# Performance work log

Measured on AMD Instinct MI355X. Metric: run time of the kernel, lower is better.

Reference implementation:

```python
import jax, jax.numpy as jnp
import numpy as np

N_NODES = 50000
N_EDGES = 800000
NODE_DIM = 128
HIDDEN = 256
LATENT = 128
COND = 5


def setup_inputs() -> dict:
    key = jax.random.key(0)
    ks = jax.random.split(key, 10)
    s = lambda d: 1.0 / np.sqrt(d)
    return {
        "node_features": jax.random.normal(ks[0], (N_NODES, NODE_DIM), jnp.float32),
        "conditions": jax.random.normal(ks[1], (COND,), jnp.float32),
        "src": jax.random.randint(ks[2], (N_EDGES,), 0, N_NODES, jnp.int32),
        "dst": jax.random.randint(ks[3], (N_EDGES,), 0, N_NODES, jnp.int32),
        "W1": jax.random.normal(ks[4], (NODE_DIM, HIDDEN), jnp.float32) * s(NODE_DIM),
        "b1": jnp.zeros((HIDDEN,), jnp.float32),
        "W2": jax.random.normal(ks[5], (HIDDEN, HIDDEN), jnp.float32) * s(HIDDEN),
        "b2": jnp.zeros((HIDDEN,), jnp.float32),
        "Wfc": jax.random.normal(ks[6], (HIDDEN + COND, LATENT), jnp.float32) * s(HIDDEN + COND),
        "bfc": jnp.zeros((LATENT,), jnp.float32),
        "Wmean": jax.random.normal(ks[7], (LATENT, LATENT), jnp.float32) * s(LATENT),
        "bmean": jnp.zeros((LATENT,), jnp.float32),
        "Wlogvar": jax.random.normal(ks[8], (LATENT, LATENT), jnp.float32) * s(LATENT),
        "blogvar": jnp.zeros((LATENT,), jnp.float32),
    }


def _graph_conv(x, src, dst, W, b, n_nodes):
    # gather source-node features along edges, sum-aggregate onto targets,
    # then linear transform: standard GraphConv (sum aggregation)
    agg = jax.ops.segment_sum(x[src], dst, num_segments=n_nodes)  # [N, d]
    return agg @ W + b


def reference(node_features, conditions, src, dst,
              W1, b1, W2, b2, Wfc, bfc, Wmean, bmean, Wlogvar, blogvar):
    n = node_features.shape[0]
    x = jax.nn.relu(_graph_conv(node_features, src, dst, W1, b1, n))  # [N, H]
    x = jax.nn.relu(_graph_conv(x, src, dst, W2, b2, n))              # [N, H]
    pooled = jnp.mean(x, axis=0)                                      # [H]
    h = jax.nn.relu(jnp.concatenate([pooled, conditions], axis=-1) @ Wfc + bfc)
    z_mean = h @ Wmean + bmean
    z_logvar = h @ Wlogvar + blogvar
    return z_mean, z_logvar
```

## Files before the change

kernel.cpp:

```cpp
#include <hip/hip_runtime.h>

#define N_NODES   50000
#define N_EDGES   800000
#define NODE_DIM  128
#define HIDDEN    256
#define LATENT    128
#define COND      5

#define NB        196
#define P1_CHUNK  4096
#define P1_GRID   ((N_EDGES + P1_CHUNK - 1) / P1_CHUNK)

typedef unsigned int uint;
typedef unsigned short ushort;
typedef unsigned char uchar;

typedef __attribute__((ext_vector_type(8))) short bf16x8;
typedef __attribute__((ext_vector_type(4))) float f32x4;

static __device__ __forceinline__ ushort f32_to_bf16(float f) {
    union { float f; uint u; } v; v.f = f;
    uint r = v.u + 0x7FFF + ((v.u >> 16) & 1);
    return (ushort)(r >> 16);
}
static __device__ __forceinline__ uint pack_bf16(float lo, float hi) {
    return (uint)f32_to_bf16(lo) | ((uint)f32_to_bf16(hi) << 16);
}

static __device__ __forceinline__ void gload_lds16(const void* g, void* l) {
    __builtin_amdgcn_global_load_lds(
        (const __attribute__((address_space(1))) unsigned int*)(unsigned long long)(uintptr_t)g,
        (__attribute__((address_space(3))) unsigned int*)(unsigned int)(uintptr_t)l,
        16, 0, 0);
}


#if __has_builtin(__builtin_amdgcn_cvt_pk_f32_fp8) && __has_builtin(__builtin_amdgcn_cvt_pk_fp8_f32)
#define HW_FP8 1
#endif

#ifndef HW_FP8
static __device__ __forceinline__ float dec1_fp8(uint b) {
    uint sgn = b & 0x80, mag = b & 0x7f;
    float v;
    if (mag >= 8) {
        union { uint u; float f; } t;
        t.u = (((mag >> 3) + 120) << 23) | ((mag & 7) << 20);
        v = t.f;
    } else {
        v = (float)mag * 0.001953125f;
    }
    return sgn ? -v : v;
}
static __device__ __forceinline__ uchar enc1_fp8(float f) {
    float a = fabsf(f);
    uint s = (f < 0.f) ? 0x80u : 0u;
    if (!(a >= 0.015625f)) {
        int q = (int)(a * 512.f + 0.5f);
        if (q > 7) q = 7;
        return (uchar)(s | (uint)q);
    }
    if (a >= 448.f) return (uchar)(s | 0x7E);
    union { float f; uint u; } t; t.f = a;
    uint e = (t.u >> 23) - 120;
    uint m = (t.u >> 20) & 7;
    uint rem = t.u & 0xFFFFF;
    uint v = (e << 3) | m;
    if (rem > 0x80000 || (rem == 0x80000 && (v & 1))) v++;
    if (v > 0x7E) v = 0x7E;
    return (uchar)(s | v);
}
#endif

static __device__ __forceinline__ void dec4_add(uint u, float* acc) {
#ifdef HW_FP8
    auto lo = __builtin_amdgcn_cvt_pk_f32_fp8((int)u, false);
    auto hi = __builtin_amdgcn_cvt_pk_f32_fp8((int)u, true);
    acc[0] += lo[0]; acc[1] += lo[1]; acc[2] += hi[0]; acc[3] += hi[1];
#else
    acc[0] += dec1_fp8(u & 0xff);
    acc[1] += dec1_fp8((u >> 8) & 0xff);
    acc[2] += dec1_fp8((u >> 16) & 0xff);
    acc[3] += dec1_fp8(u >> 24);
#endif
}
static __device__ __forceinline__ void dec2_add(uint u, float* acc) {
#ifdef HW_FP8
    auto lo = __builtin_amdgcn_cvt_pk_f32_fp8((int)u, false);
    acc[0] += lo[0]; acc[1] += lo[1];
#else
    acc[0] += dec1_fp8(u & 0xff);
    acc[1] += dec1_fp8((u >> 8) & 0xff);
#endif
}
static __device__ __forceinline__ uint enc2_fp8(float a, float b) {
#ifdef HW_FP8
    return (uint)__builtin_amdgcn_cvt_pk_fp8_f32(a, b, 0, false) & 0xFFFFu;
#else
    return (uint)enc1_fp8(a) | ((uint)enc1_fp8(b) << 8);
#endif
}
static __device__ __forceinline__ uchar enc1(float v) {
#ifdef HW_FP8
    return (uchar)(__builtin_amdgcn_cvt_pk_fp8_f32(v, v, 0, false) & 0xff);
#else
    return enc1_fp8(v);
#endif
}


#define NF4   (N_NODES * NODE_DIM / 4)
#define PREP1 (NF4 + NODE_DIM * HIDDEN)
#define PREP2 (PREP1 + HIDDEN * HIDDEN)
#define PREP3 (PREP2 + HIDDEN)
#define PREP4 (PREP3 + NB)
#define PREP5 (PREP4 + NB)
#define PREP6 (PREP5 + 1)

__global__ void prep_kernel(const float* __restrict__ nf,
                            const float* __restrict__ W1, const float* __restrict__ W2,
                            uchar* __restrict__ nf_fp8,
                            ushort* __restrict__ Wst1, ushort* __restrict__ Wst2,
                            float* __restrict__ pooled,
                            int* __restrict__ bcount, int* __restrict__ bcursor2,
                            int* __restrict__ hcnt) {
    int id = blockIdx.x * blockDim.x + threadIdx.x;
    if (id < NF4) {
        float4 v = reinterpret_cast<const float4*>(nf)[id];
        uint w = enc2_fp8(v.x, v.y) | (enc2_fp8(v.z, v.w) << 16);
        reinterpret_cast<uint*>(nf_fp8)[id] = w;
    } else if (id < PREP1) {
        int i = id - NF4;
        int k = i >> 8, c = i & 255;
        int idx = ((((k >> 5) * 16) + (((k & 31) >> 3) * 4 + (c >> 6))) * 64 + (c & 63)) * 8 + (k & 7);
        Wst1[idx] = f32_to_bf16(W1[i]);
    } else if (id < PREP2) {
        int i = id - PREP1;
        int k = i >> 8, c = i & 255;
        int idx = ((((k >> 5) * 16) + (((k & 31) >> 3) * 4 + (c >> 6))) * 64 + (c & 63)) * 8 + (k & 7);
        Wst2[idx] = f32_to_bf16(W2[i]);
    } else if (id < PREP3) {
        pooled[id - PREP2] = 0.f;
    } else if (id < PREP4) {
        bcount[id - PREP3] = 0;
    } else if (id < PREP5) {
        bcursor2[id - PREP4] = 0;
    } else if (id < PREP6) {
        hcnt[0] = 0;
    }
}


__global__ __launch_bounds__(256) void bcount_kernel(const int* __restrict__ dst,
                                                     int* __restrict__ bcount) {
    __shared__ int cnt[NB];
    const int t = threadIdx.x;
    for (int i = t; i < NB; i += 256) cnt[i] = 0;
    __syncthreads();
    const int base = blockIdx.x * P1_CHUNK;
#pragma unroll
    for (int i = 0; i < 16; ++i) {
        int e = base + i * 256 + t;
        if (e < N_EDGES) atomicAdd(&cnt[dst[e] >> 8], 1);
    }
    __syncthreads();
    for (int i = t; i < NB; i += 256)
        if (cnt[i] > 0) atomicAdd(&bcount[i], cnt[i]);
}

__global__ __launch_bounds__(256) void bwrite_kernel(const int* __restrict__ src,
                                                     const int* __restrict__ dst,
                                                     const int* __restrict__ bcount,
                                                     int* __restrict__ bcursor2,
                                                     uint* __restrict__ pair_buf) {
    __shared__ int s[256];
    __shared__ int cnt[NB];
    __shared__ int gbase[NB];
    const int t = threadIdx.x;
    s[t] = (t < NB) ? bcount[t] : 0;
    __syncthreads();
    for (int off = 1; off < 256; off <<= 1) {
        int v = (t >= off) ? s[t - off] : 0;
        __syncthreads();
        s[t] += v;
        __syncthreads();
    }
    for (int i = t; i < NB; i += 256) cnt[i] = 0;
    __syncthreads();

    const int base = blockIdx.x * P1_CHUNK;
    uint pk[16];
    int  bk[16], lr[16];
    bool ok[16];
#pragma unroll
    for (int i = 0; i < 16; ++i) {
        int e = base + i * 256 + t;
        ok[i] = e < N_EDGES;
        if (ok[i]) {
            int sv = src[e], d = dst[e];
            pk[i] = (uint)sv | ((uint)d << 16);
            bk[i] = d >> 8;
        }
    }
#pragma unroll
    for (int i = 0; i < 16; ++i)
        if (ok[i]) lr[i] = atomicAdd(&cnt[bk[i]], 1);
    __syncthreads();
    if (t < NB) {
        int c = cnt[t];
        if (c > 0) gbase[t] = ((t > 0) ? s[t - 1] : 0) + atomicAdd(&bcursor2[t], c);
    }
    __syncthreads();
#pragma unroll
    for (int i = 0; i < 16; ++i)
        if (ok[i]) pair_buf[gbase[bk[i]] + lr[i]] = pk[i];
}

__global__ __launch_bounds__(256) void csrloc_kernel(const uint* __restrict__ pair_buf,
                                                     const int* __restrict__ bcount,
                                                     int* __restrict__ offsets,
                                                     ushort* __restrict__ csr) {
    __shared__ int s[256];
    __shared__ int lcnt[256];
    __shared__ int loff[256];
    __shared__ int lcur[256];
    const int t = threadIdx.x;
    const int b = blockIdx.x;
    s[t] = (t < NB) ? bcount[t] : 0;
    __syncthreads();
    for (int off = 1; off < 256; off <<= 1) {
        int v = (t >= off) ? s[t - off] : 0;
        __syncthreads();
        s[t] += v;
        __syncthreads();
    }
    const int e0 = (b > 0) ? s[b - 1] : 0;
    const int e1 = s[b];
    lcnt[t] = 0;
    lcur[t] = 0;
    __syncthreads();

    for (int j = e0 + t; j < e1; j += 256)
        atomicAdd(&lcnt[(pair_buf[j] >> 16) & 255], 1);
    __syncthreads();

    const int myc = lcnt[t];
    s[t] = myc;
    __syncthreads();
    for (int off = 1; off < 256; off <<= 1) {
        int v = (t >= off) ? s[t - off] : 0;
        __syncthreads();
        s[t] += v;
        __syncthreads();
    }
    const int lofft = s[t] - myc;
    loff[t] = lofft;
    const int node = (b << 8) + t;
    if (node < N_NODES) offsets[node] = e0 + lofft;
    if (b == 0 && t == 0) offsets[N_NODES] = N_EDGES;
    __syncthreads();

    for (int j = e0 + t; j < e1; j += 256) {
        uint p = pair_buf[j];
        int dl = (int)(p >> 16) & 255;
        int r = atomicAdd(&lcur[dl], 1);
        csr[e0 + loff[dl] + r] = (ushort)(p & 0xFFFFu);
    }
}


template <int D>
__global__ __launch_bounds__(256) void agg_kernel(const uchar* __restrict__ x,
                                                  const int* __restrict__ offsets,
                                                  const ushort* __restrict__ csr,
                                                  ushort* __restrict__ out) {
    constexpr int BPL = D / 64;
    int node = (blockIdx.x * blockDim.x + threadIdx.x) >> 6;
    int lane = threadIdx.x & 63;
    if (node >= N_NODES) return;
    int j0 = __builtin_amdgcn_readfirstlane(offsets[node]);
    int j1 = __builtin_amdgcn_readfirstlane(offsets[node + 1]);

    float acc[BPL];
#pragma unroll
    for (int i = 0; i < BPL; ++i) acc[i] = 0.f;

    const uchar* base = x + lane * BPL;
    const int il = lane & 15;

    int idxv = (j0 + il < j1) ? (int)csr[j0 + il] : 0;

    for (int jb = j0; jb < j1; jb += 16) {
        int idxn = (jb + 16 + il < j1) ? (int)csr[jb + 16 + il] : 0;
        int n = j1 - jb; n = (n > 16) ? 16 : n;
        uint u[16];
        if (n == 16) {
#pragma unroll
            for (int i = 0; i < 16; ++i) {
                int s = __shfl(idxv, i);
                if constexpr (BPL == 4)
                    u[i] = *reinterpret_cast<const uint*>(base + (size_t)s * D);
                else
                    u[i] = *reinterpret_cast<const ushort*>(base + (size_t)s * D);
            }
#pragma unroll
            for (int i = 0; i < 16; ++i) {
                if constexpr (BPL == 4) dec4_add(u[i], acc); else dec2_add(u[i], acc);
            }
        } else {
#pragma unroll
            for (int i = 0; i < 16; ++i) {
                if (i < n) {
                    int s = __shfl(idxv, i);
                    if constexpr (BPL == 4)
                        u[i] = *reinterpret_cast<const uint*>(base + (size_t)s * D);
                    else
                        u[i] = *reinterpret_cast<const ushort*>(base + (size_t)s * D);
                }
            }
#pragma unroll
            for (int i = 0; i < 16; ++i) {
                if (i < n) {
                    if constexpr (BPL == 4) dec4_add(u[i], acc); else dec2_add(u[i], acc);
                }
            }
        }
        idxv = idxn;
    }

    if constexpr (BPL == 4) {
        uint2 o;
        o.x = pack_bf16(acc[0], acc[1]);
        o.y = pack_bf16(acc[2], acc[3]);
        *reinterpret_cast<uint2*>(out + (size_t)node * D + lane * 4) = o;
    } else {
        *reinterpret_cast<uint*>(out + (size_t)node * D + lane * 2) = pack_bf16(acc[0], acc[1]);
    }
}


template <int K, bool POOL>
__global__ __launch_bounds__(256) void gemm_res_kernel(const ushort* __restrict__ A,
                                                       const ushort* __restrict__ Wst,
                                                       const float* __restrict__ bias,
                                                       uchar* __restrict__ Xout,
                                                       float* __restrict__ pooled, int nblk,
                                                       const float* __restrict__ cond,
                                                       const float* __restrict__ Wfc,
                                                       const float* __restrict__ bfc,
                                                       const float* __restrict__ Wmean,
                                                       const float* __restrict__ bmean,
                                                       const float* __restrict__ Wlogvar,
                                                       const float* __restrict__ blogvar,
                                                       float* __restrict__ outv,
                                                       int* __restrict__ hcnt) {
    constexpr int NSTEP = K / 32;
    constexpr int WB    = NSTEP * 8 * 1024;
    constexpr int AB    = NSTEP * 4 * 1024;
    constexpr int NT    = (N_NODES + 63) / 64;
    __shared__ uchar lds[WB + 2 * AB];

    const int t    = threadIdx.x;
    const int lane = t & 63;
    const int wv   = t >> 6;
    const int fr   = lane & 15;
    const int kgl  = lane >> 4;
    const int colhalf = blockIdx.x & 1;
    const int stride  = nblk >> 1;

    const int kx = (lane & 3) ^ ((lane >> 3) & 3);

#pragma unroll
    for (int j = 0; j < NSTEP * 2; ++j) {
        const int lc = wv * (NSTEP * 2) + j;
        const int ks = lc >> 3, r = lc & 7;
        const int kg = r >> 1, ccl = r & 1;
        gload_lds16(Wst + ((size_t)ks * 16 + kg * 4 + colhalf * 2 + ccl) * 512 + lane * 8,
                    &lds[lc * 1024]);
    }

    auto stageA = [&](int buf, int row0) {
#pragma unroll
        for (int j = 0; j < NSTEP; ++j) {
            const int c  = wv * NSTEP + j;
            const int ks = c >> 2, rt = c & 3;
            gload_lds16(A + (size_t)(row0 + rt * 16 + (lane >> 2)) * K + ks * 32 + kx * 8,
                        &lds[WB + buf * AB + c * 1024]);
        }
    };

    const int rowsel = (wv & 1) * 2;
    const int colsel = wv >> 1;
    const int col0   = colhalf * 128 + colsel * 64;
    float bcol[4];
#pragma unroll
    for (int ct = 0; ct < 4; ++ct) bcol[ct] = bias[col0 + ct * 16 + fr];
    const int mrow = kgl * 4;
    const int aswz = (kgl ^ ((fr >> 1) & 3)) * 16;

    float cs[4] = {0.f, 0.f, 0.f, 0.f};

    int tile = blockIdx.x >> 1;
    stageA(0, tile * 64);
    __syncthreads();

    for (int buf = 0; tile < NT; tile += stride, buf ^= 1) {
        const int tn = tile + stride;
        if (tn < NT) stageA(buf ^ 1, tn * 64);

        f32x4 acc[2][4];
#pragma unroll
        for (int rt = 0; rt < 2; ++rt)
#pragma unroll
            for (int ct = 0; ct < 4; ++ct)
                acc[rt][ct] = (f32x4){0.f, 0.f, 0.f, 0.f};

        const uchar* ab = &lds[WB + buf * AB];
#pragma unroll
        for (int ks = 0; ks < NSTEP; ++ks) {
            bf16x8 af[2], bfv[4];
#pragma unroll
            for (int rt = 0; rt < 2; ++rt)
                af[rt] = *reinterpret_cast<const bf16x8*>(ab + (ks * 4 + rowsel + rt) * 1024 + fr * 64 + aswz);
#pragma unroll
            for (int ct = 0; ct < 4; ++ct)
                bfv[ct] = *reinterpret_cast<const bf16x8*>(&lds[(ks * 8 + kgl * 2 + colsel) * 1024 + (ct * 16 + fr) * 16]);
#pragma unroll
            for (int rt = 0; rt < 2; ++rt)
#pragma unroll
                for (int ct = 0; ct < 4; ++ct)
                    acc[rt][ct] = __builtin_amdgcn_mfma_f32_16x16x32_bf16(af[rt], bfv[ct], acc[rt][ct], 0, 0, 0);
        }

        const int rowbase = tile * 64 + (wv & 1) * 32;
        if constexpr (POOL) {
#pragma unroll
            for (int rt = 0; rt < 2; ++rt) {
#pragma unroll
                for (int e = 0; e < 4; ++e) {
                    int m = rowbase + rt * 16 + mrow + e;
                    if (m < N_NODES) {
#pragma unroll
                        for (int ct = 0; ct < 4; ++ct)
                            cs[ct] += fmaxf(acc[rt][ct][e] + bcol[ct], 0.f);
                    }
                }
            }
        } else {
#pragma unroll
            for (int rt = 0; rt < 2; ++rt) {
#pragma unroll
                for (int e = 0; e < 4; ++e) {
                    int m = rowbase + rt * 16 + mrow + e;
                    if (m < N_NODES) {
#pragma unroll
                        for (int ct = 0; ct < 4; ++ct) {
                            float v = fmaxf(acc[rt][ct][e] + bcol[ct], 0.f);
                            Xout[(size_t)m * HIDDEN + col0 + ct * 16 + fr] = enc1(v);
                        }
                    }
                }
            }
        }
        __syncthreads();
    }

    if constexpr (POOL) {
#pragma unroll
        for (int ct = 0; ct < 4; ++ct) {
            cs[ct] += __shfl_xor(cs[ct], 16);
            cs[ct] += __shfl_xor(cs[ct], 32);
        }
        if (lane < 16) {
#pragma unroll
            for (int ct = 0; ct < 4; ++ct)
                atomicAdd(&pooled[col0 + ct * 16 + lane], cs[ct]);
        }

        __threadfence();
        __shared__ int lastflag;
        if (t == 0) lastflag = (atomicAdd(hcnt, 1) == nblk - 1) ? 1 : 0;
        __syncthreads();
        if (lastflag) {
            float* hv = (float*)lds;
            float* hh = (float*)(lds + 2048);
            if (t < HIDDEN) hv[t] = atomicAdd(&pooled[t], 0.0f) * (1.0f / N_NODES);
            if (t < COND) hv[HIDDEN + t] = cond[t];
            __syncthreads();
            if (t < LATENT) {
                float s = bfc[t];
                for (int k = 0; k < HIDDEN + COND; ++k) s += hv[k] * Wfc[k * LATENT + t];
                hh[t] = fmaxf(s, 0.f);
            }
            __syncthreads();
            if (t < LATENT) {
                float s = bmean[t];
                for (int k = 0; k < LATENT; ++k) s += hh[k] * Wmean[k * LATENT + t];
                outv[t] = s;
            } else if (t < 2 * LATENT) {
                int j = t - LATENT;
                float s = blogvar[j];
                for (int k = 0; k < LATENT; ++k) s += hh[k] * Wlogvar[k * LATENT + j];
                outv[LATENT + j] = s;
            }
        }
    }
}


extern "C" void kernel_launch(void* const* d_in, const int* in_sizes, int n_in,
                              void* d_out, int out_size, void* d_ws, size_t ws_size,
                              hipStream_t stream) {
    const float* node_features = (const float*)d_in[0];
    const float* conditions    = (const float*)d_in[1];
    const int*   src           = (const int*)d_in[2];
    const int*   dst           = (const int*)d_in[3];
    const float* W1  = (const float*)d_in[4];
    const float* b1  = (const float*)d_in[5];
    const float* W2  = (const float*)d_in[6];
    const float* b2  = (const float*)d_in[7];
    const float* Wfc = (const float*)d_in[8];
    const float* bfc = (const float*)d_in[9];
    const float* Wmean   = (const float*)d_in[10];
    const float* bmean   = (const float*)d_in[11];
    const float* Wlogvar = (const float*)d_in[12];
    const float* blogvar = (const float*)d_in[13];
    float* out = (float*)d_out;

    size_t o = 0;
    auto alloc = [&](size_t bytes) {
        void* p = (char*)d_ws + o;
        o += (bytes + 255) & ~(size_t)255;
        return p;
    };
    int* offsets   = (int*)alloc((size_t)(N_NODES + 1) * 4);
    int* bcount    = (int*)alloc((size_t)NB * 4);
    int* bcursor2  = (int*)alloc((size_t)NB * 4);
    int* hcnt      = (int*)alloc(4);
    uint* pair_buf = (uint*)alloc((size_t)N_EDGES * 4);
    ushort* csr    = (ushort*)alloc((size_t)N_EDGES * 2);
    float* pooled  = (float*)alloc(HIDDEN * 4);
    ushort* Wst1   = (ushort*)alloc((size_t)HIDDEN * NODE_DIM * 2);
    ushort* Wst2   = (ushort*)alloc((size_t)HIDDEN * HIDDEN * 2);
    uchar* nf_fp8  = (uchar*)alloc((size_t)N_NODES * NODE_DIM);
    uchar* x1_fp8  = (uchar*)alloc((size_t)N_NODES * HIDDEN);
    ushort* agg1   = (ushort*)alloc((size_t)(N_NODES + 64) * NODE_DIM * 2);
    ushort* agg2   = (ushort*)alloc((size_t)(N_NODES + 64) * HIDDEN * 2);

    prep_kernel<<<(PREP6 + 255) / 256, 256, 0, stream>>>(
        node_features, W1, W2, nf_fp8, Wst1, Wst2, pooled, bcount, bcursor2, hcnt);

    bcount_kernel<<<P1_GRID, 256, 0, stream>>>(dst, bcount);
    bwrite_kernel<<<P1_GRID, 256, 0, stream>>>(src, dst, bcount, bcursor2, pair_buf);
    csrloc_kernel<<<NB, 256, 0, stream>>>(pair_buf, bcount, offsets, csr);

    const int AGG_GRID = (N_NODES * 64 + 255) / 256;
    const int G1_BLK = 512;
    const int G2_BLK = 256;

    agg_kernel<NODE_DIM><<<AGG_GRID, 256, 0, stream>>>(nf_fp8, offsets, csr, agg1);
    gemm_res_kernel<NODE_DIM, false><<<G1_BLK, 256, 0, stream>>>(
        agg1, Wst1, b1, x1_fp8, nullptr, G1_BLK,
        nullptr, nullptr, nullptr, nullptr, nullptr, nullptr, nullptr, nullptr, nullptr);

    agg_kernel<HIDDEN><<<AGG_GRID, 256, 0, stream>>>(x1_fp8, offsets, csr, agg2);
    gemm_res_kernel<HIDDEN, true><<<G2_BLK, 256, 0, stream>>>(
        agg2, Wst2, b2, nullptr, pooled, G2_BLK,
        conditions, Wfc, bfc, Wmean, bmean, Wlogvar, blogvar, out, hcnt);
}
```

Before: 150.4 us.

## Split second GEMM into quarter-column tiles with 32-row tiles and more blocks

The second GEMM+pool kernel becomes its own specialized kernel. Each block now owns a quarter of the output columns and 32-row tiles instead of half the columns and 64-row tiles, and the grid doubles to 512 blocks. This cuts per-block LDS for the weights (32KB) and raises occupancy and parallelism for the memory-bound pooled GEMM. The cost is that each A tile is loaded by four column groups instead of two. The threadfence before the completion counter is replaced by a vmcnt wait plus a barrier.

```diff
diff --git a/kernel.cpp b/kernel.cpp
--- a/kernel.cpp
+++ b/kernel.cpp
@@ -339,21 +339,11 @@
 }
 
 
-template <int K, bool POOL>
-__global__ __launch_bounds__(256) void gemm_res_kernel(const ushort* __restrict__ A,
-                                                       const ushort* __restrict__ Wst,
-                                                       const float* __restrict__ bias,
-                                                       uchar* __restrict__ Xout,
-                                                       float* __restrict__ pooled, int nblk,
-                                                       const float* __restrict__ cond,
-                                                       const float* __restrict__ Wfc,
-                                                       const float* __restrict__ bfc,
-                                                       const float* __restrict__ Wmean,
-                                                       const float* __restrict__ bmean,
-                                                       const float* __restrict__ Wlogvar,
-                                                       const float* __restrict__ blogvar,
-                                                       float* __restrict__ outv,
-                                                       int* __restrict__ hcnt) {
+__global__ __launch_bounds__(256) void gemm1_kernel(const ushort* __restrict__ A,
+                                                    const ushort* __restrict__ Wst,
+                                                    const float* __restrict__ bias,
+                                                    uchar* __restrict__ Xout, int nblk) {
+    constexpr int K = NODE_DIM;
     constexpr int NSTEP = K / 32;
     constexpr int WB    = NSTEP * 8 * 1024;
     constexpr int AB    = NSTEP * 4 * 1024;
@@ -398,8 +388,6 @@
     const int mrow = kgl * 4;
     const int aswz = (kgl ^ ((fr >> 1) & 3)) * 16;
 
-    float cs[4] = {0.f, 0.f, 0.f, 0.f};
-
     int tile = blockIdx.x >> 1;
     stageA(0, tile * 64);
     __syncthreads();
@@ -433,76 +421,157 @@
         }
 
         const int rowbase = tile * 64 + (wv & 1) * 32;
-        if constexpr (POOL) {
-#pragma unroll
-            for (int rt = 0; rt < 2; ++rt) {
-#pragma unroll
-                for (int e = 0; e < 4; ++e) {
-                    int m = rowbase + rt * 16 + mrow + e;
-                    if (m < N_NODES) {
-#pragma unroll
-                        for (int ct = 0; ct < 4; ++ct)
-                            cs[ct] += fmaxf(acc[rt][ct][e] + bcol[ct], 0.f);
+#pragma unroll
+        for (int rt = 0; rt < 2; ++rt) {
+#pragma unroll
+            for (int e = 0; e < 4; ++e) {
+                int m = rowbase + rt * 16 + mrow + e;
+                if (m < N_NODES) {
+#pragma unroll
+                    for (int ct = 0; ct < 4; ++ct) {
+                        float v = fmaxf(acc[rt][ct][e] + bcol[ct], 0.f);
+                        Xout[(size_t)m * HIDDEN + col0 + ct * 16 + fr] = enc1(v);
                     }
                 }
             }
-        } else {
-#pragma unroll
-            for (int rt = 0; rt < 2; ++rt) {
-#pragma unroll
-                for (int e = 0; e < 4; ++e) {
-                    int m = rowbase + rt * 16 + mrow + e;
-                    if (m < N_NODES) {
-#pragma unroll
-                        for (int ct = 0; ct < 4; ++ct) {
-                            float v = fmaxf(acc[rt][ct][e] + bcol[ct], 0.f);
-                            Xout[(size_t)m * HIDDEN + col0 + ct * 16 + fr] = enc1(v);
-                        }
-                    }
-                }
+        }
+        __syncthreads();
+    }
+}
+
+
+__global__ __launch_bounds__(256) void gemm2_kernel(const ushort* __restrict__ A,
+                                                    const ushort* __restrict__ Wst,
+                                                    const float* __restrict__ bias,
+                                                    float* __restrict__ pooled, int nblk,
+                                                    const float* __restrict__ cond,
+                                                    const float* __restrict__ Wfc,
+                                                    const float* __restrict__ bfc,
+                                                    const float* __restrict__ Wmean,
+                                                    const float* __restrict__ bmean,
+                                                    const float* __restrict__ Wlogvar,
+                                                    const float* __restrict__ blogvar,
+                                                    float* __restrict__ outv,
+                                                    int* __restrict__ hcnt) {
+    constexpr int K   = HIDDEN;
+    constexpr int WB  = 32768;
+    constexpr int AB  = 16384;
+    constexpr int NT  = (N_NODES + 31) / 32;
+    __shared__ uchar lds[WB + 2 * AB];
+    __shared__ int lastflag;
+
+    const int t    = threadIdx.x;
+    const int lane = t & 63;
+    const int wv   = t >> 6;
+    const int fr   = lane & 15;
+    const int kgl  = lane >> 4;
+    const int colq    = blockIdx.x & 3;
+    const int stride  = nblk >> 2;
+
+    const int kx = (lane & 3) ^ ((lane >> 3) & 3);
+
+#pragma unroll
+    for (int j = 0; j < 8; ++j) {
+        const int lc = wv * 8 + j;
+        const int ks = lc >> 2, kg = lc & 3;
+        gload_lds16(Wst + ((size_t)ks * 16 + kg * 4 + colq) * 512 + lane * 8,
+                    &lds[lc * 1024]);
+    }
+
+    auto stageA = [&](int buf, int row0) {
+#pragma unroll
+        for (int j = 0; j < 4; ++j) {
+            const int c  = wv * 4 + j;
+            const int ks = c >> 1, rh = c & 1;
+            gload_lds16(A + (size_t)(row0 + rh * 16 + (lane >> 2)) * K + ks * 32 + kx * 8,
+                        &lds[WB + buf * AB + c * 1024]);
+        }
+    };
+
+    const int rowhalf = wv & 1;
+    const int colh32  = wv >> 1;
+    const int col0    = colq * 64 + colh32 * 32;
+    float bcol[2];
+#pragma unroll
+    for (int ct = 0; ct < 2; ++ct) bcol[ct] = bias[col0 + ct * 16 + fr];
+    const int mrow = kgl * 4;
+    const int aswz = (kgl ^ ((fr >> 1) & 3)) * 16;
+
+    float cs[2] = {0.f, 0.f};
+    int tile = blockIdx.x >> 2;
+    stageA(0, tile * 32);
+    __syncthreads();
+
+    for (int buf = 0; tile < NT; tile += stride, buf ^= 1) {
+        const int tn = tile + stride;
+        if (tn < NT) stageA(buf ^ 1, tn * 32);
+
+        f32x4 acc[2];
+        acc[0] = (f32x4){0.f, 0.f, 0.f, 0.f};
+        acc[1] = (f32x4){0.f, 0.f, 0.f, 0.f};
+
+        const uchar* ab = &lds[WB + buf * AB];
+#pragma unroll
+        for (int ks = 0; ks < 8; ++ks) {
+            bf16x8 af, bfv[2];
+            af = *reinterpret_cast<const bf16x8*>(ab + (ks * 2 + rowhalf) * 1024 + fr * 64 + aswz);
+#pragma unroll
+            for (int ct = 0; ct < 2; ++ct)
+                bfv[ct] = *reinterpret_cast<const bf16x8*>(
+                    &lds[(ks * 4 + kgl) * 1024 + (colh32 * 32 + ct * 16 + fr) * 16]);
+#pragma unroll
+            for (int ct = 0; ct < 2; ++ct)
+                acc[ct] = __builtin_amdgcn_mfma_f32_16x16x32_bf16(af, bfv[ct], acc[ct], 0, 0, 0);
+        }
+
+        const int rowbase = tile * 32 + rowhalf * 16;
+#pragma unroll
+        for (int e = 0; e < 4; ++e) {
+            int m = rowbase + mrow + e;
+            if (m < N_NODES) {
+                cs[0] += fmaxf(acc[0][e] + bcol[0], 0.f);
+                cs[1] += fmaxf(acc[1][e] + bcol[1], 0.f);
             }
         }
         __syncthreads();
     }
 
-    if constexpr (POOL) {
-#pragma unroll
-        for (int ct = 0; ct < 4; ++ct) {
-            cs[ct] += __shfl_xor(cs[ct], 16);
-            cs[ct] += __shfl_xor(cs[ct], 32);
-        }
-        if (lane < 16) {
-#pragma unroll
-            for (int ct = 0; ct < 4; ++ct)
-                atomicAdd(&pooled[col0 + ct * 16 + lane], cs[ct]);
-        }
-
-        __threadfence();
-        __shared__ int lastflag;
-        if (t == 0) lastflag = (atomicAdd(hcnt, 1) == nblk - 1) ? 1 : 0;
-        __syncthreads();
-        if (lastflag) {
-            float* hv = (float*)lds;
-            float* hh = (float*)(lds + 2048);
-            if (t < HIDDEN) hv[t] = atomicAdd(&pooled[t], 0.0f) * (1.0f / N_NODES);
-            if (t < COND) hv[HIDDEN + t] = cond[t];
-            __syncthreads();
-            if (t < LATENT) {
-                float s = bfc[t];
-                for (int k = 0; k < HIDDEN + COND; ++k) s += hv[k] * Wfc[k * LATENT + t];
-                hh[t] = fmaxf(s, 0.f);
-            }
-            __syncthreads();
-            if (t < LATENT) {
-                float s = bmean[t];
-                for (int k = 0; k < LATENT; ++k) s += hh[k] * Wmean[k * LATENT + t];
-                outv[t] = s;
-            } else if (t < 2 * LATENT) {
-                int j = t - LATENT;
-                float s = blogvar[j];
-                for (int k = 0; k < LATENT; ++k) s += hh[k] * Wlogvar[k * LATENT + j];
-                outv[LATENT + j] = s;
-            }
+#pragma unroll
+    for (int ct = 0; ct < 2; ++ct) {
+        cs[ct] += __shfl_xor(cs[ct], 16);
+        cs[ct] += __shfl_xor(cs[ct], 32);
+    }
+    if (lane < 16) {
+#pragma unroll
+        for (int ct = 0; ct < 2; ++ct)
+            atomicAdd(&pooled[col0 + ct * 16 + lane], cs[ct]);
+    }
+
+    asm volatile("s_waitcnt vmcnt(0)" ::: "memory");
+    __syncthreads();
+    if (t == 0) lastflag = (atomicAdd(hcnt, 1) == nblk - 1) ? 1 : 0;
+    __syncthreads();
+    if (lastflag) {
+        float* hv = (float*)lds;
+        float* hh = (float*)(lds + 2048);
+        if (t < HIDDEN) hv[t] = atomicAdd(&pooled[t], 0.0f) * (1.0f / N_NODES);
+        if (t < COND) hv[HIDDEN + t] = cond[t];
+        __syncthreads();
+        if (t < LATENT) {
+            float s = bfc[t];
+            for (int k = 0; k < HIDDEN + COND; ++k) s += hv[k] * Wfc[k * LATENT + t];
+            hh[t] = fmaxf(s, 0.f);
+        }
+        __syncthreads();
+        if (t < LATENT) {
+            float s = bmean[t];
+            for (int k = 0; k < LATENT; ++k) s += hh[k] * Wmean[k * LATENT + t];
+            outv[t] = s;
+        } else if (t < 2 * LATENT) {
+            int j = t - LATENT;
+            float s = blogvar[j];
+            for (int k = 0; k < LATENT; ++k) s += hh[k] * Wlogvar[k * LATENT + j];
+            outv[LATENT + j] = s;
         }
     }
 }
@@ -556,15 +625,13 @@
 
     const int AGG_GRID = (N_NODES * 64 + 255) / 256;
     const int G1_BLK = 512;
-    const int G2_BLK = 256;
+    const int G2_BLK = 512;
 
     agg_kernel<NODE_DIM><<<AGG_GRID, 256, 0, stream>>>(nf_fp8, offsets, csr, agg1);
-    gemm_res_kernel<NODE_DIM, false><<<G1_BLK, 256, 0, stream>>>(
-        agg1, Wst1, b1, x1_fp8, nullptr, G1_BLK,
-        nullptr, nullptr, nullptr, nullptr, nullptr, nullptr, nullptr, nullptr, nullptr);
+    gemm1_kernel<<<G1_BLK, 256, 0, stream>>>(agg1, Wst1, b1, x1_fp8, G1_BLK);
 
     agg_kernel<HIDDEN><<<AGG_GRID, 256, 0, stream>>>(x1_fp8, offsets, csr, agg2);
-    gemm_res_kernel<HIDDEN, true><<<G2_BLK, 256, 0, stream>>>(
-        agg2, Wst2, b2, nullptr, pooled, G2_BLK,
+    gemm2_kernel<<<G2_BLK, 256, 0, stream>>>(
+        agg2, Wst2, b2, pooled, G2_BLK,
         conditions, Wfc, bfc, Wmean, bmean, Wlogvar, blogvar, out, hcnt);
 }
```

After: 143.3 us. 1.05x faster.
